# Kernel tuning notes

Measured on AMD Instinct MI355X. Metric: run time of the kernel, lower is better.

## Reference

```python
import jax, jax.numpy as jnp
import numpy as np
import math

B, S, D_IN, D_ATTN, D_HID = 4, 2048, 1024, 1024, 1024

def gelu_erf(x):
    return 0.5 * x * (1.0 + jax.lax.erf(x / math.sqrt(2.0)))

def setup_inputs() -> dict:
    key = jax.random.key(0)
    k = jax.random.split(key, 8)
    inputs = jax.random.normal(k[0], (B, S, D_IN), dtype=jnp.float32)
    attn_mask = jax.random.randint(k[1], (B, S, S), 0, 2, dtype=jnp.int32)
    sq = 1.0 / math.sqrt(D_IN)
    Wq = jax.random.normal(k[2], (D_IN, D_ATTN), dtype=jnp.float32) * sq
    bq = jnp.zeros((D_ATTN,), dtype=jnp.float32)
    Wk = jax.random.normal(k[3], (D_IN, D_ATTN), dtype=jnp.float32) * sq
    bk = jnp.zeros((D_ATTN,), dtype=jnp.float32)
    Wv = jax.random.normal(k[4], (D_IN, D_HID), dtype=jnp.float32) * sq
    bv = jnp.zeros((D_HID,), dtype=jnp.float32)
    return {"inputs": inputs, "attn_mask": attn_mask,
            "Wq": Wq, "bq": bq, "Wk": Wk, "bk": bk, "Wv": Wv, "bv": bv}

def reference(inputs, attn_mask, Wq, bq, Wk, bk, Wv, bv):
    # Q, K: [B, S, d_k]
    Q = inputs @ Wq + bq
    K = inputs @ Wk + bk
    scores = jnp.einsum('bqd,bkd->bqk', Q, K) / math.sqrt(D_ATTN)
    scores = scores + attn_mask.astype(scores.dtype) * (-1e9)
    attn = jax.nn.softmax(scores, axis=-1)
    WV = gelu_erf(inputs @ Wv + bv)           # [B, S, hidden]
    context = jnp.einsum('bqk,bkh->bqh', attn, WV)
    return (context, attn)
```

## Files before the change

kernel.cpp:

```cpp
#include <hip/hip_runtime.h>
#include <hip/hip_bf16.h>
#include <math.h>

#define B_   4
#define S_   2048
#define DIN  1024
#define DATT 1024
#define DHID 1024

typedef short bf16x8 __attribute__((ext_vector_type(8)));
typedef float f32x4  __attribute__((ext_vector_type(4)));

__device__ inline unsigned short f2bf(float f) {
    unsigned u = __float_as_uint(f);
    u += 0x7fffu + ((u >> 16) & 1u);
    return (unsigned short)(u >> 16);
}
__device__ inline float bf2f(unsigned u16) {
    return __uint_as_float(u16 << 16);
}
__device__ inline void gld16(const void* g, void* l) {
    __builtin_amdgcn_global_load_lds(
        (const __attribute__((address_space(1))) unsigned int*)g,
        (__attribute__((address_space(3))) unsigned int*)l, 16, 0, 0);
}

__global__ __launch_bounds__(256)
void xcvt_k(const float* __restrict__ x, unsigned short* __restrict__ xb)
{
    int i = blockIdx.x * 256 + threadIdx.x;
    const float4* p = (const float4*)x + (size_t)i * 2;
    float4 v0 = p[0], v1 = p[1];
    uint4 o;
    o.x = (unsigned)f2bf(v0.x) | ((unsigned)f2bf(v0.y) << 16);
    o.y = (unsigned)f2bf(v0.z) | ((unsigned)f2bf(v0.w) << 16);
    o.z = (unsigned)f2bf(v1.x) | ((unsigned)f2bf(v1.y) << 16);
    o.w = (unsigned)f2bf(v1.z) | ((unsigned)f2bf(v1.w) << 16);
    ((uint4*)xb)[i] = o;
}

__global__ __launch_bounds__(256)
void wcvt_k(const float* __restrict__ Wq, const float* __restrict__ Wk,
            const float* __restrict__ Wv, unsigned short* __restrict__ Wt)
{
    int w = blockIdx.y;
    const float* W = (w == 0) ? Wq : ((w == 1) ? Wk : Wv);
    unsigned short* D = Wt + (size_t)w * DIN * DATT;
    int t = blockIdx.x * 256 + threadIdx.x;
    int n  = t >> 6;
    int kc = (t & 63) * 16;
    unsigned short r[16];
#pragma unroll
    for (int i = 0; i < 16; ++i) r[i] = f2bf(W[(size_t)(kc + i) * DATT + n]);
    uint4 o0, o1;
    o0.x = (unsigned)r[0] | ((unsigned)r[1] << 16);  o0.y = (unsigned)r[2] | ((unsigned)r[3] << 16);
    o0.z = (unsigned)r[4] | ((unsigned)r[5] << 16);  o0.w = (unsigned)r[6] | ((unsigned)r[7] << 16);
    o1.x = (unsigned)r[8] | ((unsigned)r[9] << 16);  o1.y = (unsigned)r[10] | ((unsigned)r[11] << 16);
    o1.z = (unsigned)r[12] | ((unsigned)r[13] << 16); o1.w = (unsigned)r[14] | ((unsigned)r[15] << 16);
    *(uint4*)(D + (size_t)n * DIN + kc)     = o0;
    *(uint4*)(D + (size_t)n * DIN + kc + 8) = o1;
}

__global__ __launch_bounds__(256)
void mpack_k(const int* __restrict__ m, unsigned* __restrict__ mb)
{
    int w = blockIdx.x * 256 + threadIdx.x;
    const uint4* p = (const uint4*)(m + (size_t)w * 32);
    unsigned bits = 0;
#pragma unroll
    for (int g = 0; g < 8; ++g) {
        uint4 v = p[g];
        bits |= (v.x ? 1u : 0u) << (g * 4 + 0);
        bits |= (v.y ? 1u : 0u) << (g * 4 + 1);
        bits |= (v.z ? 1u : 0u) << (g * 4 + 2);
        bits |= (v.w ? 1u : 0u) << (g * 4 + 3);
    }
    mb[w] = bits;
}

template<int EPI>
__global__ __launch_bounds__(512, 2)
void gemmP_k(const unsigned short* __restrict__ Ap, const unsigned short* __restrict__ Bp,
             const float* __restrict__ b0, const float* __restrict__ b1,
             const float* __restrict__ b2, const unsigned* __restrict__ mbits,
             void* __restrict__ Cp, void* __restrict__ Cp2,
             int K, int lda, int ldb, int ldc,
             long aStride, long bStride, long cStride, float scale)
{
    __shared__ __align__(16) char ldsb[131072];

    const int tid  = threadIdx.x;
    const int z    = blockIdx.z;
    const int row0 = blockIdx.y * 256;
    const int col0 = blockIdx.x * 256;
    const int wid  = tid >> 6, lane = tid & 63;
    const int lr = lane & 15, lg = lane >> 4;
    const int wm = wid >> 2, wn = wid & 3;
    const int twv  = (tid & 448) * 16;
    const int sl16 = (lg ^ ((lr >> 1) & 3)) << 4;
    const int sj   = (tid & 3) ^ ((tid >> 3) & 3);

    const unsigned short* Ab = Ap + (size_t)aStride * z;
    const unsigned short* Bb = Bp + (size_t)bStride * z;

    f32x4 acc[8][4] = {};
    const int nt = K >> 6;

#define STA(kk, buf, kt) {                                                      \
    int gr0 = tid >> 2;                                                         \
    gld16(Ab + (size_t)(row0 + gr0) * lda + (kt) * 64 + (kk) * 32 + sj * 8,     \
          ldsb + (buf) * 32768 + (kk) * 16384 + twv);                           \
    gld16(Ab + (size_t)(row0 + 128 + gr0) * lda + (kt) * 64 + (kk) * 32 + sj * 8, \
          ldsb + (buf) * 32768 + (kk) * 16384 + 8192 + twv); }

#define STB(kk, buf, kt) {                                                      \
    int gr0 = tid >> 2;                                                         \
    gld16(Bb + (size_t)(col0 + gr0) * ldb + (kt) * 64 + (kk) * 32 + sj * 8,     \
          ldsb + 65536 + (buf) * 32768 + (kk) * 16384 + twv);                   \
    gld16(Bb + (size_t)(col0 + 128 + gr0) * ldb + (kt) * 64 + (kk) * 32 + sj * 8, \
          ldsb + 65536 + (buf) * 32768 + (kk) * 16384 + 8192 + twv); }

#define PH(buf, kk, mq, BV, LOADB, STG, DOVM) {                                 \
    const char* as_ = ldsb + (buf) * 32768 + (kk) * 16384;                      \
    const char* bs_ = ldsb + 65536 + (buf) * 32768 + (kk) * 16384;              \
    bf16x8 a0_, a1_, a2_, a3_;                                                  \
    a0_ = *(const bf16x8*)(as_ + (wm * 128 + (mq) * 64 +  0 + lr) * 64 + sl16); \
    a1_ = *(const bf16x8*)(as_ + (wm * 128 + (mq) * 64 + 16 + lr) * 64 + sl16); \
    a2_ = *(const bf16x8*)(as_ + (wm * 128 + (mq) * 64 + 32 + lr) * 64 + sl16); \
    a3_ = *(const bf16x8*)(as_ + (wm * 128 + (mq) * 64 + 48 + lr) * 64 + sl16); \
    if (LOADB) {                                                                \
        BV[0] = *(const bf16x8*)(bs_ + (wn * 64 +  0 + lr) * 64 + sl16);        \
        BV[1] = *(const bf16x8*)(bs_ + (wn * 64 + 16 + lr) * 64 + sl16);        \
        BV[2] = *(const bf16x8*)(bs_ + (wn * 64 + 32 + lr) * 64 + sl16);        \
        BV[3] = *(const bf16x8*)(bs_ + (wn * 64 + 48 + lr) * 64 + sl16);        \
    }                                                                           \
    STG;                                                                        \
    __builtin_amdgcn_s_barrier();                                               \
    asm volatile("s_waitcnt lgkmcnt(0)" ::: "memory");                          \
    __builtin_amdgcn_sched_barrier(0);                                          \
    __builtin_amdgcn_s_setprio(1);                                              \
    _Pragma("unroll")                                                           \
    for (int n = 0; n < 4; ++n) {                                               \
        acc[(mq)*4+0][n] = __builtin_amdgcn_mfma_f32_16x16x32_bf16(a0_, BV[n], acc[(mq)*4+0][n], 0,0,0); \
        acc[(mq)*4+1][n] = __builtin_amdgcn_mfma_f32_16x16x32_bf16(a1_, BV[n], acc[(mq)*4+1][n], 0,0,0); \
        acc[(mq)*4+2][n] = __builtin_amdgcn_mfma_f32_16x16x32_bf16(a2_, BV[n], acc[(mq)*4+2][n], 0,0,0); \
        acc[(mq)*4+3][n] = __builtin_amdgcn_mfma_f32_16x16x32_bf16(a3_, BV[n], acc[(mq)*4+3][n], 0,0,0); \
    }                                                                           \
    __builtin_amdgcn_s_setprio(0);                                              \
    DOVM;                                                                       \
    __builtin_amdgcn_s_barrier(); }

    STA(0, 0, 0); STB(0, 0, 0);
    STA(1, 0, 0); STB(1, 0, 0);
    STA(0, 1, 1); STB(0, 1, 1);
    asm volatile("s_waitcnt vmcnt(4)" ::: "memory");
    __builtin_amdgcn_s_barrier();

    for (int i = 0; i < (nt >> 1); ++i) {
        int t1 = 2 * i + 1;
        int t2 = 2 * i + 2; if (t2 > nt - 1) t2 = nt - 1;
        int t3 = 2 * i + 3; if (t3 > nt - 1) t3 = nt - 1;
        bf16x8 bv0[4], bv1[4];
        PH(0, 0, 0, bv0, true,  { STA(1, 1, t1); }, {})
        PH(0, 0, 1, bv0, false, { STB(1, 1, t1); }, { asm volatile("s_waitcnt vmcnt(8)" ::: "memory"); })
        PH(0, 1, 0, bv1, true,  { STA(0, 0, t2); }, {})
        PH(0, 1, 1, bv1, false, { STB(0, 0, t2); }, { asm volatile("s_waitcnt vmcnt(8)" ::: "memory"); })
        PH(1, 0, 0, bv0, true,  { STA(1, 0, t2); }, {})
        PH(1, 0, 1, bv0, false, { STB(1, 0, t2); }, { asm volatile("s_waitcnt vmcnt(8)" ::: "memory"); })
        PH(1, 1, 0, bv1, true,  { STA(0, 1, t3); }, {})
        PH(1, 1, 1, bv1, false, { STB(0, 1, t3); }, { asm volatile("s_waitcnt vmcnt(8)" ::: "memory"); })
    }
#undef PH
#undef STA
#undef STB

    if (EPI == 6) {
        int w = col0 >> 10;
        int cb0 = (col0 & 1023) + wn * 64;
        if (w < 2) {
            unsigned short* C = (unsigned short*)Cp + (size_t)w * ((size_t)B_ * S_ * DATT);
            const float* bias = w ? b1 : b0;
#pragma unroll
            for (int ni = 0; ni < 4; ++ni) {
                int col = cb0 + ni * 16 + lr;
                float bb = bias[col];
#pragma unroll
                for (int mi = 0; mi < 8; ++mi) {
                    int rowb = row0 + wm * 128 + mi * 16 + lg * 4;
#pragma unroll
                    for (int v = 0; v < 4; ++v)
                        C[(size_t)(rowb + v) * DATT + col] = f2bf(acc[mi][ni][v] + bb);
                }
            }
        } else {
            unsigned short* C = (unsigned short*)Cp2;
            int zz = row0 >> 11;
            int sb = (row0 & 2047) + wm * 128;
#pragma unroll
            for (int ni = 0; ni < 4; ++ni) {
                int col = cb0 + ni * 16 + lr;
                float bb = b2[col];
#pragma unroll
                for (int mi = 0; mi < 8; ++mi) {
                    unsigned short r[4];
#pragma unroll
                    for (int v = 0; v < 4; ++v) {
                        float xv = acc[mi][ni][v] + bb;
                        xv = 0.5f * xv * (1.0f + erff(xv * 0.70710678118654752f));
                        r[v] = f2bf(xv);
                    }
                    uint2 o;
                    o.x = (unsigned)r[0] | ((unsigned)r[1] << 16);
                    o.y = (unsigned)r[2] | ((unsigned)r[3] << 16);
                    *(uint2*)(C + ((size_t)zz * DHID + col) * S_ + sb + mi * 16 + lg * 4) = o;
                }
            }
        }
    } else {
        unsigned short* C = (unsigned short*)Cp + (size_t)cStride * z;
        const unsigned* mb = mbits + (size_t)z * (S_ * S_ / 32);
        const int wbase = (col0 + wn * 64) >> 5;
#pragma unroll
        for (int mi = 0; mi < 8; ++mi) {
            int rowb = row0 + wm * 128 + mi * 16 + lg * 4;
#pragma unroll
            for (int v = 0; v < 4; ++v) {
                int row = rowb + v;
                unsigned w0 = mb[(size_t)row * (S_ / 32) + wbase];
                unsigned w1 = mb[(size_t)row * (S_ / 32) + wbase + 1];
#pragma unroll
                for (int ni = 0; ni < 4; ++ni) {
                    int col = col0 + wn * 64 + ni * 16 + lr;
                    unsigned wsel = (ni & 2) ? w1 : w0;
                    float ev = ((wsel >> ((ni & 1) * 16 + lr)) & 1)
                             ? 0.0f : __expf(acc[mi][ni][v] * scale);
                    C[(size_t)row * ldc + col] = f2bf(ev);
                }
            }
        }
    }
}

template<int AMODE, int EPI>
__global__ __launch_bounds__(256)
void gemm_k(const void* __restrict__ Ap, const unsigned short* __restrict__ Bp,
            const float* __restrict__ b0, const float* __restrict__ b1,
            const float* __restrict__ b2, const int* __restrict__ maskp,
            void* __restrict__ Cp, void* __restrict__ Cp2,
            int K, int lda, int ldb, int ldc,
            long aStride, long bStride, long cStride, long mStride, float scale)
{
    __shared__ __align__(16) unsigned short sh[2][2][128][64];
    const int tid  = threadIdx.x;
    const int z    = blockIdx.z;
    const int row0 = blockIdx.y * 128;
    const int col0 = blockIdx.x * 128;
    const int wave = tid >> 6, lane = tid & 63;
    const int lr = lane & 15, lg = lane >> 4;
    const int wm = (wave >> 1) * 64, wn = (wave & 1) * 64;
    const unsigned short* Bb = Bp + (size_t)bStride * z;
    f32x4 acc[4][4] = {};
    const int nt = K >> 6;
    auto stage = [&](int b, int k0) {
        if (AMODE == 0) {
            const unsigned short* A = (const unsigned short*)Ap + (size_t)aStride * z;
#pragma unroll
            for (int q = 0; q < 4; ++q) {
                int c = q * 256 + tid;
                int row = c >> 3, j = c & 7;
                gld16((const char*)(A + (size_t)(row0 + row) * lda + k0) + ((j ^ (row & 7)) << 4),
                      (char*)&sh[b][0][0][0] + ((q * 256 + (tid & 192)) << 4));
            }
        } else {
            const float* A = (const float*)Ap + (size_t)aStride * z;
#pragma unroll
            for (int q = 0; q < 4; ++q) {
                int c = q * 256 + tid;
                int row = c >> 3, j = c & 7;
                const float* src = A + (size_t)(row0 + row) * lda + k0 + ((j ^ (row & 7)) << 3);
                float4 v0 = *(const float4*)src;
                float4 v1 = *(const float4*)(src + 4);
                uint4 p;
                p.x = (unsigned)f2bf(v0.x) | ((unsigned)f2bf(v0.y) << 16);
                p.y = (unsigned)f2bf(v0.z) | ((unsigned)f2bf(v0.w) << 16);
                p.z = (unsigned)f2bf(v1.x) | ((unsigned)f2bf(v1.y) << 16);
                p.w = (unsigned)f2bf(v1.z) | ((unsigned)f2bf(v1.w) << 16);
                *(uint4*)((char*)&sh[b][0][0][0] + ((size_t)c << 4)) = p;
            }
        }
#pragma unroll
        for (int q = 0; q < 4; ++q) {
            int c = q * 256 + tid;
            int row = c >> 3, j = c & 7;
            gld16((const char*)(Bb + (size_t)(col0 + row) * ldb + k0) + ((j ^ (row & 7)) << 4),
                  (char*)&sh[b][1][0][0] + ((q * 256 + (tid & 192)) << 4));
        }
    };
    stage(0, 0);
    __syncthreads();
    int cur = 0;
    for (int t = 0; t < nt; ++t) {
        if (t + 1 < nt) stage(cur ^ 1, (t + 1) << 6);
        const char* baseA = (const char*)&sh[cur][0][0][0];
        const char* baseB = (const char*)&sh[cur][1][0][0];
        bf16x8 af[2][4], bfv[2][4];
#pragma unroll
        for (int s = 0; s < 2; ++s)
#pragma unroll
            for (int i = 0; i < 4; ++i) {
                int ra = wm + i * 16 + lr;
                af[s][i]  = *(const bf16x8*)(baseA + ra * 128 + ((((s << 2) | lg) ^ (ra & 7)) << 4));
                int rb = wn + i * 16 + lr;
                bfv[s][i] = *(const bf16x8*)(baseB + rb * 128 + ((((s << 2) | lg) ^ (rb & 7)) << 4));
            }
#pragma unroll
        for (int s = 0; s < 2; ++s)
#pragma unroll
            for (int mi = 0; mi < 4; ++mi)
#pragma unroll
                for (int ni = 0; ni < 4; ++ni)
                    acc[mi][ni] = __builtin_amdgcn_mfma_f32_16x16x32_bf16(af[s][mi], bfv[s][ni], acc[mi][ni], 0, 0, 0);
        if (t + 1 < nt) __syncthreads();
        cur ^= 1;
    }
    if (EPI == 6) {
        int w = col0 >> 10;
        int cb = (col0 & 1023) + wn;
        if (w < 2) {
            unsigned short* C = (unsigned short*)Cp + (size_t)w * ((size_t)B_ * S_ * DATT);
            const float* bias = w ? b1 : b0;
#pragma unroll
            for (int mi = 0; mi < 4; ++mi)
#pragma unroll
                for (int ni = 0; ni < 4; ++ni) {
                    int col = cb + ni * 16 + lr;
                    float bb = bias[col];
                    int rowb = row0 + wm + mi * 16 + lg * 4;
#pragma unroll
                    for (int v = 0; v < 4; ++v)
                        C[(size_t)(rowb + v) * DATT + col] = f2bf(acc[mi][ni][v] + bb);
                }
        } else {
            unsigned short* C = (unsigned short*)Cp2;
            int zz = row0 >> 11;
            int sb = (row0 & 2047) + wm;
#pragma unroll
            for (int mi = 0; mi < 4; ++mi)
#pragma unroll
                for (int ni = 0; ni < 4; ++ni) {
                    int col = cb + ni * 16 + lr;
                    float bb = b2[col];
                    unsigned short r[4];
#pragma unroll
                    for (int v = 0; v < 4; ++v) {
                        float xv = acc[mi][ni][v] + bb;
                        xv = 0.5f * xv * (1.0f + erff(xv * 0.70710678118654752f));
                        r[v] = f2bf(xv);
                    }
                    uint2 o;
                    o.x = (unsigned)r[0] | ((unsigned)r[1] << 16);
                    o.y = (unsigned)r[2] | ((unsigned)r[3] << 16);
                    *(uint2*)(C + ((size_t)zz * DHID + col) * S_ + sb + mi * 16 + lg * 4) = o;
                }
        }
    } else if (EPI == 5) {
        float* C = (float*)Cp + (size_t)cStride * z;
        const float* invs = b0 + (size_t)z * S_;
#pragma unroll
        for (int mi = 0; mi < 4; ++mi)
#pragma unroll
            for (int ni = 0; ni < 4; ++ni) {
                int col = col0 + wn + ni * 16 + lr;
                int rowb = row0 + wm + mi * 16 + lg * 4;
#pragma unroll
                for (int v = 0; v < 4; ++v)
                    C[(size_t)(rowb + v) * ldc + col] = acc[mi][ni][v] * invs[rowb + v];
            }
    } else {
        float* C = (float*)Cp + (size_t)cStride * z;
        const int* mp = (EPI == 2) ? (maskp + (size_t)mStride * z) : nullptr;
#pragma unroll
        for (int mi = 0; mi < 4; ++mi)
#pragma unroll
            for (int ni = 0; ni < 4; ++ni) {
                int col = col0 + wn + ni * 16 + lr;
                int rowb = row0 + wm + mi * 16 + lg * 4;
#pragma unroll
                for (int v = 0; v < 4; ++v) {
                    float val = acc[mi][ni][v];
                    if (EPI == 2) val = val * scale + (float)mp[(size_t)(rowb + v) * ldc + col] * (-1e9f);
                    C[(size_t)(rowb + v) * ldc + col] = val;
                }
            }
    }
}

template<bool WRITEATTN>
__global__ __launch_bounds__(256)
void rownorm_k(const unsigned short* __restrict__ e, float* __restrict__ attn,
               float* __restrict__ invs)
{
    const int row = blockIdx.x;
    const int tid = threadIdx.x;
    uint4 u = ((const uint4*)(e + (size_t)row * S_))[tid];
    float f[8];
    f[0] = bf2f(u.x & 0xffffu); f[1] = bf2f(u.x >> 16);
    f[2] = bf2f(u.y & 0xffffu); f[3] = bf2f(u.y >> 16);
    f[4] = bf2f(u.z & 0xffffu); f[5] = bf2f(u.z >> 16);
    f[6] = bf2f(u.w & 0xffffu); f[7] = bf2f(u.w >> 16);
    float s = ((f[0] + f[1]) + (f[2] + f[3])) + ((f[4] + f[5]) + (f[6] + f[7]));
#pragma unroll
    for (int o = 32; o; o >>= 1) s += __shfl_xor(s, o);
    __shared__ float red[4];
    if ((tid & 63) == 0) red[tid >> 6] = s;
    __syncthreads();
    s = (red[0] + red[1]) + (red[2] + red[3]);
    float inv = 1.0f / s;
    if (WRITEATTN) {
        float* p = attn + (size_t)row * S_;
        ((float4*)p)[tid * 2]     = make_float4(f[0] * inv, f[1] * inv, f[2] * inv, f[3] * inv);
        ((float4*)p)[tid * 2 + 1] = make_float4(f[4] * inv, f[5] * inv, f[6] * inv, f[7] * inv);
    } else {
        if (tid == 0) invs[row] = inv;
    }
}

__global__ __launch_bounds__(256)
void softmax_k(float* __restrict__ attn)
{
    const int row = blockIdx.x;
    float* p = attn + (size_t)row * S_;
    const int tid = threadIdx.x;
    float4 a = ((const float4*)p)[tid * 2];
    float4 b = ((const float4*)p)[tid * 2 + 1];
    float m = fmaxf(fmaxf(fmaxf(a.x, a.y), fmaxf(a.z, a.w)),
                    fmaxf(fmaxf(b.x, b.y), fmaxf(b.z, b.w)));
#pragma unroll
    for (int o = 32; o; o >>= 1) m = fmaxf(m, __shfl_xor(m, o));
    __shared__ float redm[4];
    __shared__ float reds[4];
    if ((tid & 63) == 0) redm[tid >> 6] = m;
    __syncthreads();
    m = fmaxf(fmaxf(redm[0], redm[1]), fmaxf(redm[2], redm[3]));
    float e[8];
    e[0] = expf(a.x - m); e[1] = expf(a.y - m); e[2] = expf(a.z - m); e[3] = expf(a.w - m);
    e[4] = expf(b.x - m); e[5] = expf(b.y - m); e[6] = expf(b.z - m); e[7] = expf(b.w - m);
    float s = e[0] + e[1] + e[2] + e[3] + e[4] + e[5] + e[6] + e[7];
#pragma unroll
    for (int o = 32; o; o >>= 1) s += __shfl_xor(s, o);
    if ((tid & 63) == 0) reds[tid >> 6] = s;
    __syncthreads();
    s = reds[0] + reds[1] + reds[2] + reds[3];
    float inv = 1.0f / s;
    ((float4*)p)[tid * 2]     = make_float4(e[0] * inv, e[1] * inv, e[2] * inv, e[3] * inv);
    ((float4*)p)[tid * 2 + 1] = make_float4(e[4] * inv, e[5] * inv, e[6] * inv, e[7] * inv);
}

extern "C" void kernel_launch(void* const* d_in, const int* in_sizes, int n_in,
                              void* d_out, int out_size, void* d_ws, size_t ws_size,
                              hipStream_t stream)
{
    const float* x    = (const float*)d_in[0];
    const int*   mask = (const int*)d_in[1];
    const float* Wq   = (const float*)d_in[2];
    const float* bq   = (const float*)d_in[3];
    const float* Wk   = (const float*)d_in[4];
    const float* bk   = (const float*)d_in[5];
    const float* Wv   = (const float*)d_in[6];
    const float* bv   = (const float*)d_in[7];

    float* ctx  = (float*)d_out;
    float* attn = ctx + (size_t)B_ * S_ * DHID;

    unsigned short* Qb = (unsigned short*)ctx;
    unsigned short* Kb = Qb + (size_t)B_ * S_ * DATT;
    unsigned short* Xb   = (unsigned short*)attn;
    unsigned short* Wb   = Xb + (size_t)B_ * S_ * DIN;
    unsigned short* WVbT = Wb + (size_t)3 * DIN * DATT;

    const size_t eElems = (size_t)B_ * S_ * S_;
    const size_t mWords = (size_t)B_ * S_ * S_ / 32;
    bool fast = ws_size >= eElems * 2 + (size_t)B_ * S_ * 4 + mWords * 4 + 256;

    dim3 blk(256), blk5(512);

    xcvt_k<<<dim3(4096), blk, 0, stream>>>(x, Xb);
    wcvt_k<<<dim3(256, 3), blk, 0, stream>>>(Wq, Wk, Wv, Wb);

    if (fast) {
        unsigned short* e    = (unsigned short*)d_ws;
        float*          invs = (float*)(e + eElems);
        unsigned*       mb   = (unsigned*)(invs + (size_t)B_ * S_);

        mpack_k<<<dim3(mWords / 256), blk, 0, stream>>>(mask, mb);
        gemmP_k<6><<<dim3(12, 32, 1), blk5, 0, stream>>>(
            Xb, Wb, bq, bk, bv, nullptr, Qb, WVbT,
            DIN, DIN, DIN, 0, 0, 0, 0, 1.0f);
        gemmP_k<4><<<dim3(8, 8, 4), blk5, 0, stream>>>(
            Qb, Kb, nullptr, nullptr, nullptr, mb, e, nullptr,
            DATT, DATT, DATT, S_,
            (long)S_ * DATT, (long)S_ * DATT, (long)S_ * S_, 0.03125f);
        rownorm_k<false><<<dim3(B_ * S_), blk, 0, stream>>>(e, nullptr, invs);
        gemm_k<0, 5><<<dim3(8, 16, 4), blk, 0, stream>>>(
            e, WVbT, invs, nullptr, nullptr, nullptr, ctx, nullptr,
            S_, S_, S_, DHID,
            (long)S_ * S_, (long)DHID * S_, (long)S_ * DHID, 0, 1.0f);
        rownorm_k<true><<<dim3(B_ * S_), blk, 0, stream>>>(e, attn, nullptr);
    } else {
        unsigned short* WVw = (unsigned short*)d_ws;
        gemm_k<0, 6><<<dim3(24, 64, 1), blk, 0, stream>>>(
            Xb, Wb, bq, bk, bv, nullptr, Qb, WVw,
            DIN, DIN, DIN, 0, 0, 0, 0, 0, 1.0f);
        gemm_k<0, 2><<<dim3(16, 16, 4), blk, 0, stream>>>(
            Qb, Kb, nullptr, nullptr, nullptr, mask, attn, nullptr,
            DATT, DATT, DATT, S_,
            (long)S_ * DATT, (long)S_ * DATT, (long)S_ * S_, (long)S_ * S_, 0.03125f);
        softmax_k<<<dim3(B_ * S_), blk, 0, stream>>>(attn);
        gemm_k<1, 3><<<dim3(8, 16, 4), blk, 0, stream>>>(
            attn, WVw, nullptr, nullptr, nullptr, nullptr, ctx, nullptr,
            S_, S_, S_, DHID,
            (long)S_ * S_, (long)DHID * S_, (long)S_ * DHID, 0, 1.0f);
    }
}
```

Measured before the change: 240.4 us.

## Replace pipelined 256x256 GEMM with simpler 256x128 tile, add block swizzle, fuse rownorm

Swaps the hand-pipelined double-buffered 256x256 GEMM for a simpler single-buffered 256x128 tile kernel with XOR-swizzled LDS. It also raises the occupancy bound to 4 blocks and adds an XCD-aware block-index swizzle to both GEMM kernels. A new workspace tier moves WV into the workspace, so attn is written once in a combined normalization pass before the context GEMM instead of in a second rownorm pass. The simpler GEMM gives up the overlap of loads and compute, which it tries to recover through occupancy, and it depends on the workspace being large enough.

Result: faster. 215.3 us (-10.4%).

```diff
diff --git a/kernel.cpp b/kernel.cpp
--- a/kernel.cpp
+++ b/kernel.cpp
@@ -23,6 +23,17 @@
     __builtin_amdgcn_global_load_lds(
         (const __attribute__((address_space(1))) unsigned int*)g,
         (__attribute__((address_space(3))) unsigned int*)l, 16, 0, 0);
+}
+__device__ inline void xswz(int& bx, int& by, int& bz)
+{
+    int gx = gridDim.x, gy = gridDim.y, gz = gridDim.z;
+    int nwg = gx * gy * gz;
+    int lin = blockIdx.x + gx * (blockIdx.y + gy * blockIdx.z);
+    int swz = (nwg & 7) ? lin : ((lin & 7) * (nwg >> 3) + (lin >> 3));
+    bx = swz % gx;
+    int t = swz / gx;
+    by = t % gy;
+    bz = t / gy;
 }
 
 __global__ __launch_bounds__(256)
@@ -79,100 +90,68 @@
 }
 
 template<int EPI>
-__global__ __launch_bounds__(512, 2)
-void gemmP_k(const unsigned short* __restrict__ Ap, const unsigned short* __restrict__ Bp,
+__global__ __launch_bounds__(512, 4)
+void gemmS_k(const unsigned short* __restrict__ Ap, const unsigned short* __restrict__ Bp,
              const float* __restrict__ b0, const float* __restrict__ b1,
              const float* __restrict__ b2, const unsigned* __restrict__ mbits,
              void* __restrict__ Cp, void* __restrict__ Cp2,
              int K, int lda, int ldb, int ldc,
              long aStride, long bStride, long cStride, float scale)
 {
-    __shared__ __align__(16) char ldsb[131072];
-
+    __shared__ __align__(16) unsigned short Al[256][64];
+    __shared__ __align__(16) unsigned short Bl[128][64];
+
+    int bx, by, z;
+    xswz(bx, by, z);
     const int tid  = threadIdx.x;
-    const int z    = blockIdx.z;
-    const int row0 = blockIdx.y * 256;
-    const int col0 = blockIdx.x * 256;
+    const int row0 = by * 256;
+    const int col0 = bx * 128;
     const int wid  = tid >> 6, lane = tid & 63;
     const int lr = lane & 15, lg = lane >> 4;
-    const int wm = wid >> 2, wn = wid & 3;
-    const int twv  = (tid & 448) * 16;
-    const int sl16 = (lg ^ ((lr >> 1) & 3)) << 4;
-    const int sj   = (tid & 3) ^ ((tid >> 3) & 3);
+    const int wm = wid >> 1, wn = wid & 1;
+    const int wb = (tid & 448) * 16;
 
     const unsigned short* Ab = Ap + (size_t)aStride * z;
     const unsigned short* Bb = Bp + (size_t)bStride * z;
 
-    f32x4 acc[8][4] = {};
+    f32x4 acc[4][4] = {};
     const int nt = K >> 6;
 
-#define STA(kk, buf, kt) {                                                      \
-    int gr0 = tid >> 2;                                                         \
-    gld16(Ab + (size_t)(row0 + gr0) * lda + (kt) * 64 + (kk) * 32 + sj * 8,     \
-          ldsb + (buf) * 32768 + (kk) * 16384 + twv);                           \
-    gld16(Ab + (size_t)(row0 + 128 + gr0) * lda + (kt) * 64 + (kk) * 32 + sj * 8, \
-          ldsb + (buf) * 32768 + (kk) * 16384 + 8192 + twv); }
-
-#define STB(kk, buf, kt) {                                                      \
-    int gr0 = tid >> 2;                                                         \
-    gld16(Bb + (size_t)(col0 + gr0) * ldb + (kt) * 64 + (kk) * 32 + sj * 8,     \
-          ldsb + 65536 + (buf) * 32768 + (kk) * 16384 + twv);                   \
-    gld16(Bb + (size_t)(col0 + 128 + gr0) * ldb + (kt) * 64 + (kk) * 32 + sj * 8, \
-          ldsb + 65536 + (buf) * 32768 + (kk) * 16384 + 8192 + twv); }
-
-#define PH(buf, kk, mq, BV, LOADB, STG, DOVM) {                                 \
-    const char* as_ = ldsb + (buf) * 32768 + (kk) * 16384;                      \
-    const char* bs_ = ldsb + 65536 + (buf) * 32768 + (kk) * 16384;              \
-    bf16x8 a0_, a1_, a2_, a3_;                                                  \
-    a0_ = *(const bf16x8*)(as_ + (wm * 128 + (mq) * 64 +  0 + lr) * 64 + sl16); \
-    a1_ = *(const bf16x8*)(as_ + (wm * 128 + (mq) * 64 + 16 + lr) * 64 + sl16); \
-    a2_ = *(const bf16x8*)(as_ + (wm * 128 + (mq) * 64 + 32 + lr) * 64 + sl16); \
-    a3_ = *(const bf16x8*)(as_ + (wm * 128 + (mq) * 64 + 48 + lr) * 64 + sl16); \
-    if (LOADB) {                                                                \
-        BV[0] = *(const bf16x8*)(bs_ + (wn * 64 +  0 + lr) * 64 + sl16);        \
-        BV[1] = *(const bf16x8*)(bs_ + (wn * 64 + 16 + lr) * 64 + sl16);        \
-        BV[2] = *(const bf16x8*)(bs_ + (wn * 64 + 32 + lr) * 64 + sl16);        \
-        BV[3] = *(const bf16x8*)(bs_ + (wn * 64 + 48 + lr) * 64 + sl16);        \
-    }                                                                           \
-    STG;                                                                        \
-    __builtin_amdgcn_s_barrier();                                               \
-    asm volatile("s_waitcnt lgkmcnt(0)" ::: "memory");                          \
-    __builtin_amdgcn_sched_barrier(0);                                          \
-    __builtin_amdgcn_s_setprio(1);                                              \
-    _Pragma("unroll")                                                           \
-    for (int n = 0; n < 4; ++n) {                                               \
-        acc[(mq)*4+0][n] = __builtin_amdgcn_mfma_f32_16x16x32_bf16(a0_, BV[n], acc[(mq)*4+0][n], 0,0,0); \
-        acc[(mq)*4+1][n] = __builtin_amdgcn_mfma_f32_16x16x32_bf16(a1_, BV[n], acc[(mq)*4+1][n], 0,0,0); \
-        acc[(mq)*4+2][n] = __builtin_amdgcn_mfma_f32_16x16x32_bf16(a2_, BV[n], acc[(mq)*4+2][n], 0,0,0); \
-        acc[(mq)*4+3][n] = __builtin_amdgcn_mfma_f32_16x16x32_bf16(a3_, BV[n], acc[(mq)*4+3][n], 0,0,0); \
-    }                                                                           \
-    __builtin_amdgcn_s_setprio(0);                                              \
-    DOVM;                                                                       \
-    __builtin_amdgcn_s_barrier(); }
-
-    STA(0, 0, 0); STB(0, 0, 0);
-    STA(1, 0, 0); STB(1, 0, 0);
-    STA(0, 1, 1); STB(0, 1, 1);
-    asm volatile("s_waitcnt vmcnt(4)" ::: "memory");
-    __builtin_amdgcn_s_barrier();
-
-    for (int i = 0; i < (nt >> 1); ++i) {
-        int t1 = 2 * i + 1;
-        int t2 = 2 * i + 2; if (t2 > nt - 1) t2 = nt - 1;
-        int t3 = 2 * i + 3; if (t3 > nt - 1) t3 = nt - 1;
-        bf16x8 bv0[4], bv1[4];
-        PH(0, 0, 0, bv0, true,  { STA(1, 1, t1); }, {})
-        PH(0, 0, 1, bv0, false, { STB(1, 1, t1); }, { asm volatile("s_waitcnt vmcnt(8)" ::: "memory"); })
-        PH(0, 1, 0, bv1, true,  { STA(0, 0, t2); }, {})
-        PH(0, 1, 1, bv1, false, { STB(0, 0, t2); }, { asm volatile("s_waitcnt vmcnt(8)" ::: "memory"); })
-        PH(1, 0, 0, bv0, true,  { STA(1, 0, t2); }, {})
-        PH(1, 0, 1, bv0, false, { STB(1, 0, t2); }, { asm volatile("s_waitcnt vmcnt(8)" ::: "memory"); })
-        PH(1, 1, 0, bv1, true,  { STA(0, 1, t3); }, {})
-        PH(1, 1, 1, bv1, false, { STB(0, 1, t3); }, { asm volatile("s_waitcnt vmcnt(8)" ::: "memory"); })
-    }
-#undef PH
-#undef STA
-#undef STB
+    const int srow = tid >> 3, sj = tid & 7;
+
+    for (int t = 0; t < nt; ++t) {
+        const int k0 = t << 6;
+#pragma unroll
+        for (int r = 0; r < 4; ++r) {
+            int row = r * 64 + srow;
+            gld16(Ab + (size_t)(row0 + row) * lda + k0 + ((sj ^ (row & 7)) << 3),
+                  (char*)&Al[0][0] + r * 8192 + wb);
+        }
+#pragma unroll
+        for (int r = 0; r < 2; ++r) {
+            int row = r * 64 + srow;
+            gld16(Bb + (size_t)(col0 + row) * ldb + k0 + ((sj ^ (row & 7)) << 3),
+                  (char*)&Bl[0][0] + r * 8192 + wb);
+        }
+        __syncthreads();
+#pragma unroll
+        for (int s = 0; s < 2; ++s) {
+            bf16x8 av[4], bv[4];
+#pragma unroll
+            for (int i = 0; i < 4; ++i) {
+                int ra = wm * 64 + i * 16 + lr;
+                av[i] = *(const bf16x8*)((const char*)&Al[0][0] + ra * 128 + ((((s << 2) | lg) ^ (ra & 7)) << 4));
+                int rb = wn * 64 + i * 16 + lr;
+                bv[i] = *(const bf16x8*)((const char*)&Bl[0][0] + rb * 128 + ((((s << 2) | lg) ^ (rb & 7)) << 4));
+            }
+#pragma unroll
+            for (int mi = 0; mi < 4; ++mi)
+#pragma unroll
+                for (int ni = 0; ni < 4; ++ni)
+                    acc[mi][ni] = __builtin_amdgcn_mfma_f32_16x16x32_bf16(av[mi], bv[ni], acc[mi][ni], 0, 0, 0);
+        }
+        __syncthreads();
+    }
 
     if (EPI == 6) {
         int w = col0 >> 10;
@@ -185,8 +164,8 @@
                 int col = cb0 + ni * 16 + lr;
                 float bb = bias[col];
 #pragma unroll
-                for (int mi = 0; mi < 8; ++mi) {
-                    int rowb = row0 + wm * 128 + mi * 16 + lg * 4;
+                for (int mi = 0; mi < 4; ++mi) {
+                    int rowb = row0 + wm * 64 + mi * 16 + lg * 4;
 #pragma unroll
                     for (int v = 0; v < 4; ++v)
                         C[(size_t)(rowb + v) * DATT + col] = f2bf(acc[mi][ni][v] + bb);
@@ -195,13 +174,13 @@
         } else {
             unsigned short* C = (unsigned short*)Cp2;
             int zz = row0 >> 11;
-            int sb = (row0 & 2047) + wm * 128;
+            int sb = (row0 & 2047) + wm * 64;
 #pragma unroll
             for (int ni = 0; ni < 4; ++ni) {
                 int col = cb0 + ni * 16 + lr;
                 float bb = b2[col];
 #pragma unroll
-                for (int mi = 0; mi < 8; ++mi) {
+                for (int mi = 0; mi < 4; ++mi) {
                     unsigned short r[4];
 #pragma unroll
                     for (int v = 0; v < 4; ++v) {
@@ -221,8 +200,8 @@
         const unsigned* mb = mbits + (size_t)z * (S_ * S_ / 32);
         const int wbase = (col0 + wn * 64) >> 5;
 #pragma unroll
-        for (int mi = 0; mi < 8; ++mi) {
-            int rowb = row0 + wm * 128 + mi * 16 + lg * 4;
+        for (int mi = 0; mi < 4; ++mi) {
+            int rowb = row0 + wm * 64 + mi * 16 + lg * 4;
 #pragma unroll
             for (int v = 0; v < 4; ++v) {
                 int row = rowb + v;
@@ -251,10 +230,11 @@
             long aStride, long bStride, long cStride, long mStride, float scale)
 {
     __shared__ __align__(16) unsigned short sh[2][2][128][64];
+    int bx, by, z;
+    xswz(bx, by, z);
     const int tid  = threadIdx.x;
-    const int z    = blockIdx.z;
-    const int row0 = blockIdx.y * 128;
-    const int col0 = blockIdx.x * 128;
+    const int row0 = by * 128;
+    const int col0 = bx * 128;
     const int wave = tid >> 6, lane = tid & 63;
     const int lr = lane & 15, lg = lane >> 4;
     const int wm = (wave >> 1) * 64, wn = (wave & 1) * 64;
@@ -395,6 +375,32 @@
     }
 }
 
+__global__ __launch_bounds__(256)
+void rownormM_k(const unsigned short* __restrict__ e, float* __restrict__ attn,
+                float* __restrict__ invs)
+{
+    const int row = blockIdx.x;
+    const int tid = threadIdx.x;
+    uint4 u = ((const uint4*)(e + (size_t)row * S_))[tid];
+    float f[8];
+    f[0] = bf2f(u.x & 0xffffu); f[1] = bf2f(u.x >> 16);
+    f[2] = bf2f(u.y & 0xffffu); f[3] = bf2f(u.y >> 16);
+    f[4] = bf2f(u.z & 0xffffu); f[5] = bf2f(u.z >> 16);
+    f[6] = bf2f(u.w & 0xffffu); f[7] = bf2f(u.w >> 16);
+    float s = ((f[0] + f[1]) + (f[2] + f[3])) + ((f[4] + f[5]) + (f[6] + f[7]));
+#pragma unroll
+    for (int o = 32; o; o >>= 1) s += __shfl_xor(s, o);
+    __shared__ float red[4];
+    if ((tid & 63) == 0) red[tid >> 6] = s;
+    __syncthreads();
+    s = (red[0] + red[1]) + (red[2] + red[3]);
+    float inv = 1.0f / s;
+    float* p = attn + (size_t)row * S_;
+    ((float4*)p)[tid * 2]     = make_float4(f[0] * inv, f[1] * inv, f[2] * inv, f[3] * inv);
+    ((float4*)p)[tid * 2 + 1] = make_float4(f[4] * inv, f[5] * inv, f[6] * inv, f[7] * inv);
+    if (tid == 0) invs[row] = inv;
+}
+
 template<bool WRITEATTN>
 __global__ __launch_bounds__(256)
 void rownorm_k(const unsigned short* __restrict__ e, float* __restrict__ attn,
@@ -474,29 +480,51 @@
 
     unsigned short* Qb = (unsigned short*)ctx;
     unsigned short* Kb = Qb + (size_t)B_ * S_ * DATT;
-    unsigned short* Xb   = (unsigned short*)attn;
-    unsigned short* Wb   = Xb + (size_t)B_ * S_ * DIN;
-    unsigned short* WVbT = Wb + (size_t)3 * DIN * DATT;
-
-    const size_t eElems = (size_t)B_ * S_ * S_;
-    const size_t mWords = (size_t)B_ * S_ * S_ / 32;
-    bool fast = ws_size >= eElems * 2 + (size_t)B_ * S_ * 4 + mWords * 4 + 256;
+    unsigned short* Xb = (unsigned short*)attn;
+    unsigned short* Wb = Xb + (size_t)B_ * S_ * DIN;
+
+    const size_t eElems  = (size_t)B_ * S_ * S_;
+    const size_t mWords  = eElems / 32;
+    const size_t wvElems = (size_t)B_ * DHID * S_;
+
+    size_t needFast = eElems * 2 + (size_t)B_ * S_ * 4 + mWords * 4 + wvElems * 2 + 256;
+    size_t needMid  = eElems * 2 + (size_t)B_ * S_ * 4 + mWords * 4 + 256;
 
     dim3 blk(256), blk5(512);
 
     xcvt_k<<<dim3(4096), blk, 0, stream>>>(x, Xb);
     wcvt_k<<<dim3(256, 3), blk, 0, stream>>>(Wq, Wk, Wv, Wb);
 
-    if (fast) {
+    if (ws_size >= needFast) {
         unsigned short* e    = (unsigned short*)d_ws;
         float*          invs = (float*)(e + eElems);
         unsigned*       mb   = (unsigned*)(invs + (size_t)B_ * S_);
+        unsigned short* WVbT = (unsigned short*)(mb + mWords);
 
         mpack_k<<<dim3(mWords / 256), blk, 0, stream>>>(mask, mb);
-        gemmP_k<6><<<dim3(12, 32, 1), blk5, 0, stream>>>(
+        gemmS_k<6><<<dim3(24, 32, 1), blk5, 0, stream>>>(
             Xb, Wb, bq, bk, bv, nullptr, Qb, WVbT,
             DIN, DIN, DIN, 0, 0, 0, 0, 1.0f);
-        gemmP_k<4><<<dim3(8, 8, 4), blk5, 0, stream>>>(
+        gemmS_k<4><<<dim3(16, 8, 4), blk5, 0, stream>>>(
+            Qb, Kb, nullptr, nullptr, nullptr, mb, e, nullptr,
+            DATT, DATT, DATT, S_,
+            (long)S_ * DATT, (long)S_ * DATT, (long)S_ * S_, 0.03125f);
+        rownormM_k<<<dim3(B_ * S_), blk, 0, stream>>>(e, attn, invs);
+        gemm_k<0, 5><<<dim3(8, 16, 4), blk, 0, stream>>>(
+            e, WVbT, invs, nullptr, nullptr, nullptr, ctx, nullptr,
+            S_, S_, S_, DHID,
+            (long)S_ * S_, (long)DHID * S_, (long)S_ * DHID, 0, 1.0f);
+    } else if (ws_size >= needMid) {
+        unsigned short* e    = (unsigned short*)d_ws;
+        float*          invs = (float*)(e + eElems);
+        unsigned*       mb   = (unsigned*)(invs + (size_t)B_ * S_);
+        unsigned short* WVbT = Wb + (size_t)3 * DIN * DATT;
+
+        mpack_k<<<dim3(mWords / 256), blk, 0, stream>>>(mask, mb);
+        gemmS_k<6><<<dim3(24, 32, 1), blk5, 0, stream>>>(
+            Xb, Wb, bq, bk, bv, nullptr, Qb, WVbT,
+            DIN, DIN, DIN, 0, 0, 0, 0, 1.0f);
+        gemmS_k<4><<<dim3(16, 8, 4), blk5, 0, stream>>>(
             Qb, Kb, nullptr, nullptr, nullptr, mb, e, nullptr,
             DATT, DATT, DATT, S_,
             (long)S_ * DATT, (long)S_ * DATT, (long)S_ * S_, 0.03125f);
```
